# Optimization experiments

Hardware: AMD Instinct MI355X
Metric: run time of the kernel (lower is better)

Reference implementation:

```python
import jax, jax.numpy as jnp
import numpy as np

D_MODEL = 512
NUM_HEADS = 8


def setup_inputs() -> dict:
    key = jax.random.key(0)
    ks = jax.random.split(key, 12)
    B, S, D = 2, 4096, D_MODEL
    scale = 1.0 / np.sqrt(D)
    inp = {
        "q": jax.random.normal(ks[0], (B, S, D), jnp.float32),
        "k": jax.random.normal(ks[1], (B, S, D), jnp.float32),
        "v": jax.random.normal(ks[2], (B, S, D), jnp.float32),
        "w_q": jax.random.normal(ks[3], (D, D), jnp.float32) * scale,
        "b_q": jax.random.normal(ks[4], (D,), jnp.float32) * scale,
        "w_k": jax.random.normal(ks[5], (D, D), jnp.float32) * scale,
        "b_k": jax.random.normal(ks[6], (D,), jnp.float32) * scale,
        "w_v": jax.random.normal(ks[7], (D, D), jnp.float32) * scale,
        "b_v": jax.random.normal(ks[8], (D,), jnp.float32) * scale,
        "w_o": jax.random.normal(ks[9], (D, D), jnp.float32) * scale,
        "b_o": jax.random.normal(ks[10], (D,), jnp.float32) * scale,
    }
    return inp


def _split_heads(x, h):
    b, s, d = x.shape
    return x.reshape(b, s, h, d // h).transpose(0, 2, 1, 3)  # [B,H,S,dk]


def reference(q, k, v, w_q, b_q, w_k, b_k, w_v, b_v, w_o, b_o):
    h = NUM_HEADS
    # Linear projections (torch Linear: x @ W.T + b)
    qh = _split_heads(q @ w_q.T + b_q, h)
    kh = _split_heads(k @ w_k.T + b_k, h)
    vh = _split_heads(v @ w_v.T + b_v, h)
    d_k = kh.shape[-1]
    scores = jnp.einsum("bhsd,bhtd->bhst", qh, kh) / jnp.sqrt(jnp.float32(d_k))
    attn = jax.nn.softmax(scores, axis=-1)  # [B,H,S,S] - materialized, as in source
    out = jnp.einsum("bhst,bhtd->bhsd", attn, vh)
    b, _, s, dk = out.shape
    out = out.transpose(0, 2, 1, 3).reshape(b, s, h * dk)
    return out @ w_o.T + b_o
```

## Files before the change

### kernel.cpp

```cpp
#include <hip/hip_runtime.h>
#include <hip/hip_bf16.h>

#define D_MODEL 512
#define NHEAD   8
#define DK      64
#define SEQ     4096
#define BATCH   2
#define NTOK    (BATCH * SEQ)

typedef __bf16 bf16;
typedef __bf16 bf16x2 __attribute__((ext_vector_type(2)));
typedef __bf16 bf16x4 __attribute__((ext_vector_type(4)));
typedef __bf16 bf16x8 __attribute__((ext_vector_type(8)));
typedef float  f32x4  __attribute__((ext_vector_type(4)));
typedef float  f32x16 __attribute__((ext_vector_type(16)));
typedef unsigned u32x4 __attribute__((ext_vector_type(4)));

#define MFMA16(a, b, c) __builtin_amdgcn_mfma_f32_16x16x32_bf16((a), (b), (c), 0, 0, 0)
#define MFMA32(a, b, c) __builtin_amdgcn_mfma_f32_32x32x16_bf16((a), (b), (c), 0, 0, 0)

#define QSCALE 0.18033688f

__device__ __forceinline__ unsigned pkbf16(float a, float b) {
    bf16x2 t = {(bf16)a, (bf16)b};
    return __builtin_bit_cast(unsigned, t);
}

__device__ __forceinline__ void softmax_pack(const f32x16& sc, float& l,
                                             u32x4& pa, u32x4& pb) {
    float p0 = __builtin_amdgcn_exp2f(sc[0]);
    float p1 = __builtin_amdgcn_exp2f(sc[1]);
    float p2 = __builtin_amdgcn_exp2f(sc[2]);
    float p3 = __builtin_amdgcn_exp2f(sc[3]);
    l += (p0 + p1) + (p2 + p3);
    unsigned y0 = pkbf16(p0, p1), y1 = pkbf16(p2, p3);
    p0 = __builtin_amdgcn_exp2f(sc[4]);
    p1 = __builtin_amdgcn_exp2f(sc[5]);
    p2 = __builtin_amdgcn_exp2f(sc[6]);
    p3 = __builtin_amdgcn_exp2f(sc[7]);
    l += (p0 + p1) + (p2 + p3);
    unsigned y2 = pkbf16(p0, p1), y3 = pkbf16(p2, p3);
    auto s0 = __builtin_amdgcn_permlane32_swap(y0, y2, false, false);
    auto s1 = __builtin_amdgcn_permlane32_swap(y1, y3, false, false);
    pa[0] = s0[0]; pa[2] = s0[1]; pa[1] = s1[0]; pa[3] = s1[1];

    p0 = __builtin_amdgcn_exp2f(sc[8]);
    p1 = __builtin_amdgcn_exp2f(sc[9]);
    p2 = __builtin_amdgcn_exp2f(sc[10]);
    p3 = __builtin_amdgcn_exp2f(sc[11]);
    l += (p0 + p1) + (p2 + p3);
    y0 = pkbf16(p0, p1); y1 = pkbf16(p2, p3);
    p0 = __builtin_amdgcn_exp2f(sc[12]);
    p1 = __builtin_amdgcn_exp2f(sc[13]);
    p2 = __builtin_amdgcn_exp2f(sc[14]);
    p3 = __builtin_amdgcn_exp2f(sc[15]);
    l += (p0 + p1) + (p2 + p3);
    y2 = pkbf16(p0, p1); y3 = pkbf16(p2, p3);
    auto s2 = __builtin_amdgcn_permlane32_swap(y0, y2, false, false);
    auto s3 = __builtin_amdgcn_permlane32_swap(y1, y3, false, false);
    pb[0] = s2[0]; pb[2] = s2[1]; pb[1] = s3[0]; pb[3] = s3[1];
}

__global__ __launch_bounds__(256) void cvt_w(
    const float* __restrict__ wq, const float* __restrict__ wk,
    const float* __restrict__ wv, const float* __restrict__ wo,
    bf16* __restrict__ Wb)
{
    int i = blockIdx.x * 256 + threadIdx.x;
    int m = i >> 16;
    int g = i & 65535;
    const float* src = (m == 0) ? wq : (m == 1) ? wk : (m == 2) ? wv : wo;
    float4 x = *(const float4*)(src + (size_t)g * 4);
    bf16x4 y = {(bf16)x.x, (bf16)x.y, (bf16)x.z, (bf16)x.w};
    *(bf16x4*)(Wb + (size_t)m * D_MODEL * D_MODEL + (size_t)g * 4) = y;
}

__global__ __launch_bounds__(256, 3) void proj_qkv(
    const float* __restrict__ q, const float* __restrict__ k, const float* __restrict__ v,
    const bf16* __restrict__ Wb,
    const float* __restrict__ bq, const float* __restrict__ bk, const float* __restrict__ bv,
    bf16* __restrict__ Qh, bf16* __restrict__ Kh, bf16* __restrict__ Vt)
{
    const int p = blockIdx.z;
    const float* X    = (p == 0) ? q  : (p == 1) ? k  : v;
    const bf16*  W    = Wb + (size_t)p * D_MODEL * D_MODEL;
    const float* bias = (p == 0) ? bq : (p == 1) ? bk : bv;

    __shared__ union __align__(16) {
        struct { bf16 As[128][72]; bf16 Bs[128][72]; } g;
        bf16 T[128][136];
    } sm;

    const int m0   = blockIdx.x * 128;
    const int n0   = blockIdx.y * 128;
    const int tid  = threadIdx.x;
    const int lane = tid & 63;
    const int wave = tid >> 6;
    const int low4 = lane & 15;
    const int quad = lane >> 4;
    const int wm   = wave >> 1;
    const int wn   = wave & 1;

    int srow[8], sc4[8];
    for (int it = 0; it < 8; ++it) {
        int idx = tid + it * 256;
        srow[it] = idx >> 4;
        sc4[it]  = (idx & 15) * 4;
    }
    int br[4], bc[4];
    for (int it = 0; it < 4; ++it) {
        int idx = tid + it * 256;
        br[it] = idx >> 3;
        bc[it] = (idx & 7) * 8;
    }

    float4 gA[8];
    bf16x8 gB[4];
    for (int it = 0; it < 8; ++it)
        gA[it] = *(const float4*)(X + (size_t)(m0 + srow[it]) * D_MODEL + sc4[it]);
    for (int it = 0; it < 4; ++it)
        gB[it] = *(const bf16x8*)(W + (size_t)(n0 + br[it]) * D_MODEL + bc[it]);

    f32x4 acc[4][4];
    for (int i = 0; i < 4; ++i)
        for (int j = 0; j < 4; ++j)
            acc[i][j] = f32x4{0.f, 0.f, 0.f, 0.f};

    for (int k0 = 0; k0 < D_MODEL; k0 += 64) {
        __syncthreads();
        for (int it = 0; it < 8; ++it) {
            bf16x4 wa = {(bf16)gA[it].x, (bf16)gA[it].y, (bf16)gA[it].z, (bf16)gA[it].w};
            *(bf16x4*)&sm.g.As[srow[it]][sc4[it]] = wa;
        }
        for (int it = 0; it < 4; ++it)
            *(bf16x8*)&sm.g.Bs[br[it]][bc[it]] = gB[it];
        __syncthreads();

        if (k0 + 64 < D_MODEL) {
            for (int it = 0; it < 8; ++it)
                gA[it] = *(const float4*)(X + (size_t)(m0 + srow[it]) * D_MODEL + k0 + 64 + sc4[it]);
            for (int it = 0; it < 4; ++it)
                gB[it] = *(const bf16x8*)(W + (size_t)(n0 + br[it]) * D_MODEL + k0 + 64 + bc[it]);
        }

        for (int ks = 0; ks < 2; ++ks) {
            bf16x8 a[4], b[4];
            for (int i = 0; i < 4; ++i)
                a[i] = *(const bf16x8*)&sm.g.As[wm * 64 + i * 16 + low4][ks * 32 + quad * 8];
            for (int j = 0; j < 4; ++j)
                b[j] = *(const bf16x8*)&sm.g.Bs[wn * 64 + j * 16 + low4][ks * 32 + quad * 8];
            for (int i = 0; i < 4; ++i)
                for (int j = 0; j < 4; ++j)
                    acc[i][j] = MFMA16(a[i], b[j], acc[i][j]);
        }
    }

    if (p < 2) {
        bf16* Out = (p == 0) ? Qh : Kh;
        const float sc = (p == 0) ? QSCALE : 1.0f;
        for (int j = 0; j < 4; ++j) {
            int col = n0 + wn * 64 + j * 16 + low4;
            float bcol = bias[col];
            for (int i = 0; i < 4; ++i)
                for (int r = 0; r < 4; ++r) {
                    int row = m0 + wm * 64 + i * 16 + quad * 4 + r;
                    Out[(size_t)row * D_MODEL + col] = (bf16)((acc[i][j][r] + bcol) * sc);
                }
        }
    } else {
        __syncthreads();
        for (int j = 0; j < 4; ++j) {
            int col = n0 + wn * 64 + j * 16 + low4;
            float bcol = bias[col];
            for (int i = 0; i < 4; ++i)
                for (int r = 0; r < 4; ++r)
                    sm.T[wn * 64 + j * 16 + low4][wm * 64 + i * 16 + quad * 4 + r] =
                        (bf16)(acc[i][j][r] + bcol);
        }
        __syncthreads();
        const int bb = m0 >> 12;
        const int s0 = (m0 & 4095);
        for (int it = 0; it < 8; ++it) {
            int cc = it * 16 + (tid >> 4);
            int ml = (tid & 15) * 8;
            int col = n0 + cc;
            int hh = col >> 6, dd = col & 63;
            *(bf16x8*)&Vt[(((size_t)(bb * NHEAD + hh) * DK + dd) << 12) + s0 + ml] =
                *(const bf16x8*)&sm.T[cc][ml];
        }
    }
}

__global__ __launch_bounds__(512, 2) void attn(
    const bf16* __restrict__ Qh, const bf16* __restrict__ Kh,
    const bf16* __restrict__ Vt, bf16* __restrict__ O)
{
    __shared__ union __align__(16) {
        struct { bf16 Ks[2][128][72]; bf16 Vs[2][64][136]; } s;
        float Obuf[4][32][68];
    } sm;
    __shared__ float Lbuf[4][32];

    const int q0   = blockIdx.x * 256;
    const int bh   = blockIdx.y;
    const int b    = bh >> 3, h = bh & 7;
    const int tid  = threadIdx.x;
    const int lane = tid & 63;
    const int wave = tid >> 6;
    const int qg   = wave >> 1;
    const int kg   = wave & 1;
    const int m32  = lane & 31;
    const int hl   = lane >> 5;

    const bf16* Kbase = Kh + (size_t)b * SEQ * D_MODEL + h * DK;
    const bf16* Vbase = Vt + (size_t)bh * DK * SEQ;

    const bf16* Qrow0 = Qh + (size_t)(b * SEQ + q0 + qg * 64 + m32) * D_MODEL + h * DK;
    const bf16* Qrow1 = Qrow0 + (size_t)32 * D_MODEL;
    bf16x8 qf0[4], qf1[4];
#pragma unroll
    for (int ks = 0; ks < 4; ++ks) {
        qf0[ks] = *(const bf16x8*)(Qrow0 + ks * 16 + hl * 8);
        qf1[ks] = *(const bf16x8*)(Qrow1 + ks * 16 + hl * 8);
    }

    float l0 = 0.f, l1 = 0.f;
    f32x16 acc00, acc01, acc10, acc11;
#pragma unroll
    for (int i = 0; i < 16; ++i) {
        acc00[i] = 0.f; acc01[i] = 0.f; acc10[i] = 0.f; acc11[i] = 0.f;
    }

    int kr[2], kc[2], vr[2], vc[2];
#pragma unroll
    for (int it = 0; it < 2; ++it) {
        int c = tid + it * 512;
        kr[it] = c >> 3;  kc[it] = (c & 7) * 8;
        vr[it] = c >> 4;  vc[it] = (c & 15) * 8;
    }
    bf16x8 gk[2], gv[2];
#pragma unroll
    for (int it = 0; it < 2; ++it) {
        gk[it] = *(const bf16x8*)(Kbase + (size_t)kr[it] * D_MODEL + kc[it]);
        gv[it] = *(const bf16x8*)(Vbase + (size_t)vr[it] * SEQ + vc[it]);
    }
#pragma unroll
    for (int it = 0; it < 2; ++it) {
        *(bf16x8*)&sm.s.Ks[0][kr[it]][kc[it]] = gk[it];
        *(bf16x8*)&sm.s.Vs[0][vr[it]][vc[it]] = gv[it];
    }

    for (int t0 = 0; t0 < SEQ; t0 += 128) {
        const int cur = (t0 >> 7) & 1;
        const bool pf = (t0 + 128 < SEQ);

        if (pf) {
#pragma unroll
            for (int it = 0; it < 2; ++it) {
                gk[it] = *(const bf16x8*)(Kbase + (size_t)(t0 + 128 + kr[it]) * D_MODEL + kc[it]);
                gv[it] = *(const bf16x8*)(Vbase + (size_t)vr[it] * SEQ + t0 + 128 + vc[it]);
            }
        }

        __syncthreads();

        u32x4 pq0[4], pq1[4];
#pragma unroll
        for (int mt = 0; mt < 2; ++mt) {
            f32x16 s0, s1;
#pragma unroll
            for (int i = 0; i < 16; ++i) { s0[i] = 0.f; s1[i] = 0.f; }
            __builtin_amdgcn_s_setprio(1);
#pragma unroll
            for (int ks = 0; ks < 4; ++ks) {
                bf16x8 kf = *(const bf16x8*)&sm.s.Ks[cur][kg * 64 + mt * 32 + m32][ks * 16 + hl * 8];
                s0 = MFMA32(kf, qf0[ks], s0);
                s1 = MFMA32(kf, qf1[ks], s1);
            }
            __builtin_amdgcn_s_setprio(0);
            u32x4 a0, b0, a1, b1;
            softmax_pack(s0, l0, a0, b0);
            softmax_pack(s1, l1, a1, b1);
            pq0[2 * mt] = a0; pq0[2 * mt + 1] = b0;
            pq1[2 * mt] = a1; pq1[2 * mt + 1] = b1;
        }

        __builtin_amdgcn_s_setprio(1);
#pragma unroll
        for (int ksl = 0; ksl < 4; ++ksl) {
            bf16x8 pA = __builtin_bit_cast(bf16x8, pq0[ksl]);
            bf16x8 pB = __builtin_bit_cast(bf16x8, pq1[ksl]);
            bf16x8 v0 = *(const bf16x8*)&sm.s.Vs[cur][0 * 32 + m32][kg * 64 + ksl * 16 + hl * 8];
            acc00 = MFMA32(pA, v0, acc00);
            acc10 = MFMA32(pB, v0, acc10);
            bf16x8 v1 = *(const bf16x8*)&sm.s.Vs[cur][1 * 32 + m32][kg * 64 + ksl * 16 + hl * 8];
            acc01 = MFMA32(pA, v1, acc01);
            acc11 = MFMA32(pB, v1, acc11);
        }
        __builtin_amdgcn_s_setprio(0);

        if (pf) {
#pragma unroll
            for (int it = 0; it < 2; ++it) {
                *(bf16x8*)&sm.s.Ks[cur ^ 1][kr[it]][kc[it]] = gk[it];
                *(bf16x8*)&sm.s.Vs[cur ^ 1][vr[it]][vc[it]] = gv[it];
            }
        }
    }

    l0 += __shfl_xor(l0, 32);
    l1 += __shfl_xor(l1, 32);

#pragma unroll
    for (int qs = 0; qs < 2; ++qs) {
        float l = (qs == 0) ? l0 : l1;
        __syncthreads();
        if (kg == 1) {
#pragma unroll
            for (int r = 0; r < 16; ++r) {
                int qq = (r & 3) + 8 * (r >> 2) + 4 * hl;
                sm.Obuf[qg][qq][0 * 32 + m32] = (qs == 0) ? acc00[r] : acc10[r];
                sm.Obuf[qg][qq][1 * 32 + m32] = (qs == 0) ? acc01[r] : acc11[r];
            }
            if (hl == 0) Lbuf[qg][m32] = l;
        }
        __syncthreads();
        if (kg == 0) {
            float lt  = l + Lbuf[qg][m32];
            float inv = 1.0f / lt;
#pragma unroll
            for (int r = 0; r < 16; ++r) {
                int qq = (r & 3) + 8 * (r >> 2) + 4 * hl;
                float v0 = ((qs == 0) ? acc00[r] : acc10[r]) + sm.Obuf[qg][qq][0 * 32 + m32];
                float v1 = ((qs == 0) ? acc01[r] : acc11[r]) + sm.Obuf[qg][qq][1 * 32 + m32];
                float iv = __shfl(inv, qq);
                size_t row = (size_t)(b * SEQ + q0 + qg * 64 + qs * 32 + qq);
                O[row * D_MODEL + h * DK + 0 * 32 + m32] = (bf16)(v0 * iv);
                O[row * D_MODEL + h * DK + 1 * 32 + m32] = (bf16)(v1 * iv);
            }
        }
    }
}

__global__ __launch_bounds__(256, 4) void proj_out(
    const bf16* __restrict__ Oin, const bf16* __restrict__ Wo,
    const float* __restrict__ bo, float* __restrict__ out)
{
    __shared__ bf16 As[64][72];
    __shared__ bf16 Bs[64][72];

    const int m0   = blockIdx.x * 64;
    const int n0   = blockIdx.y * 64;
    const int tid  = threadIdx.x;
    const int lane = tid & 63;
    const int wave = tid >> 6;
    const int low4 = lane & 15;
    const int quad = lane >> 4;
    const int wm   = wave >> 1;
    const int wn   = wave & 1;

    int arow[2], ag[2];
    for (int it = 0; it < 2; ++it) {
        int idx = tid + it * 256;
        arow[it] = idx >> 3;
        ag[it]   = (idx & 7) * 8;
    }

    bf16x8 gA[2], gB[2];
    for (int it = 0; it < 2; ++it) {
        gA[it] = *(const bf16x8*)(Oin + (size_t)(m0 + arow[it]) * D_MODEL + ag[it]);
        gB[it] = *(const bf16x8*)(Wo + (size_t)(n0 + arow[it]) * D_MODEL + ag[it]);
    }

    f32x4 acc[2][2];
    for (int i = 0; i < 2; ++i)
        for (int j = 0; j < 2; ++j)
            acc[i][j] = f32x4{0.f, 0.f, 0.f, 0.f};

    for (int k0 = 0; k0 < D_MODEL; k0 += 64) {
        __syncthreads();
        for (int it = 0; it < 2; ++it) {
            *(bf16x8*)&As[arow[it]][ag[it]] = gA[it];
            *(bf16x8*)&Bs[arow[it]][ag[it]] = gB[it];
        }
        __syncthreads();

        if (k0 + 64 < D_MODEL) {
            for (int it = 0; it < 2; ++it) {
                gA[it] = *(const bf16x8*)(Oin + (size_t)(m0 + arow[it]) * D_MODEL + k0 + 64 + ag[it]);
                gB[it] = *(const bf16x8*)(Wo + (size_t)(n0 + arow[it]) * D_MODEL + k0 + 64 + ag[it]);
            }
        }

        for (int ks = 0; ks < 2; ++ks) {
            bf16x8 a[2], b[2];
            for (int i = 0; i < 2; ++i)
                a[i] = *(const bf16x8*)&As[wm * 32 + i * 16 + low4][ks * 32 + quad * 8];
            for (int j = 0; j < 2; ++j)
                b[j] = *(const bf16x8*)&Bs[wn * 32 + j * 16 + low4][ks * 32 + quad * 8];
            for (int i = 0; i < 2; ++i)
                for (int j = 0; j < 2; ++j)
                    acc[i][j] = MFMA16(a[i], b[j], acc[i][j]);
        }
    }

    for (int j = 0; j < 2; ++j) {
        int col = n0 + wn * 32 + j * 16 + low4;
        float bcol = bo[col];
        for (int i = 0; i < 2; ++i)
            for (int r = 0; r < 4; ++r) {
                int row = m0 + wm * 32 + i * 16 + quad * 4 + r;
                out[(size_t)row * D_MODEL + col] = acc[i][j][r] + bcol;
            }
    }
}

extern "C" void kernel_launch(void* const* d_in, const int* in_sizes, int n_in,
                              void* d_out, int out_size, void* d_ws, size_t ws_size,
                              hipStream_t stream)
{
    const float* q  = (const float*)d_in[0];
    const float* k  = (const float*)d_in[1];
    const float* v  = (const float*)d_in[2];
    const float* wq = (const float*)d_in[3];
    const float* bq = (const float*)d_in[4];
    const float* wk = (const float*)d_in[5];
    const float* bk = (const float*)d_in[6];
    const float* wv = (const float*)d_in[7];
    const float* bv = (const float*)d_in[8];
    const float* wo = (const float*)d_in[9];
    const float* bo = (const float*)d_in[10];

    const size_t NT = (size_t)NTOK * D_MODEL;
    bf16* Qh = (bf16*)d_ws;
    bf16* Kh = Qh + NT;
    bf16* Vt = Kh + NT;
    bf16* O  = Vt + NT;
    bf16* Wb = O + NT;

    cvt_w<<<1024, 256, 0, stream>>>(wq, wk, wv, wo, Wb);

    dim3 g1(NTOK / 128, D_MODEL / 128, 3);
    proj_qkv<<<g1, 256, 0, stream>>>(q, k, v, Wb, bq, bk, bv, Qh, Kh, Vt);

    dim3 g2(SEQ / 256, BATCH * NHEAD);
    attn<<<g2, 512, 0, stream>>>(Qh, Kh, Vt, O);

    dim3 g3(NTOK / 64, D_MODEL / 64);
    proj_out<<<g3, 256, 0, stream>>>(O, Wb + (size_t)3 * D_MODEL * D_MODEL, bo, (float*)d_out);
}
```

Measured before the change: 220.3 us.

## Software-pipeline PV MMA one tile behind QK with triple-buffered LDS

Restructures the attention main loop so the P·V MFMAs for the previous key tile run before the QK^T and softmax of the current tile, letting matrix work overlap softmax VALU work. K/V shared buffers go from double to triple so the previous V tile stays resident while the next is being filled, and a final epilogue drains the last PV step. Launch bounds drop to one 512-thread block per CU, since LDS usage and the extra live P registers grow. This risks lower occupancy and less latency hiding across blocks.

```diff
diff --git a/kernel.cpp b/kernel.cpp
--- a/kernel.cpp
+++ b/kernel.cpp
@@ -191,12 +191,12 @@
     }
 }
 
-__global__ __launch_bounds__(512, 2) void attn(
+__global__ __launch_bounds__(512, 1) void attn(
     const bf16* __restrict__ Qh, const bf16* __restrict__ Kh,
     const bf16* __restrict__ Vt, bf16* __restrict__ O)
 {
     __shared__ union __align__(16) {
-        struct { bf16 Ks[2][128][72]; bf16 Vs[2][64][136]; } s;
+        struct { bf16 Ks[3][128][72]; bf16 Vs[3][64][136]; } s;
         float Obuf[4][32][68];
     } sm;
     __shared__ float Lbuf[4][32];
@@ -231,6 +231,10 @@
         acc00[i] = 0.f; acc01[i] = 0.f; acc10[i] = 0.f; acc11[i] = 0.f;
     }
 
+    u32x4 pc0[4], pc1[4];
+#pragma unroll
+    for (int i = 0; i < 4; ++i) { pc0[i] = u32x4{0,0,0,0}; pc1[i] = u32x4{0,0,0,0}; }
+
     int kr[2], kc[2], vr[2], vc[2];
 #pragma unroll
     for (int it = 0; it < 2; ++it) {
@@ -250,9 +254,12 @@
         *(bf16x8*)&sm.s.Vs[0][vr[it]][vc[it]] = gv[it];
     }
 
+    int bi = 0;
     for (int t0 = 0; t0 < SEQ; t0 += 128) {
-        const int cur = (t0 >> 7) & 1;
-        const bool pf = (t0 + 128 < SEQ);
+        const int nbi = (bi == 2) ? 0 : bi + 1;
+        const int pbi = (bi == 0) ? 2 : bi - 1;
+        const bool pf    = (t0 + 128 < SEQ);
+        const bool first = (t0 == 0);
 
         if (pf) {
 #pragma unroll
@@ -264,7 +271,22 @@
 
         __syncthreads();
 
-        u32x4 pq0[4], pq1[4];
+        if (!first) {
+            __builtin_amdgcn_s_setprio(1);
+#pragma unroll
+            for (int ksl = 0; ksl < 4; ++ksl) {
+                bf16x8 pA = __builtin_bit_cast(bf16x8, pc0[ksl]);
+                bf16x8 pB = __builtin_bit_cast(bf16x8, pc1[ksl]);
+                bf16x8 v0 = *(const bf16x8*)&sm.s.Vs[pbi][0 * 32 + m32][kg * 64 + ksl * 16 + hl * 8];
+                acc00 = MFMA32(pA, v0, acc00);
+                acc10 = MFMA32(pB, v0, acc10);
+                bf16x8 v1 = *(const bf16x8*)&sm.s.Vs[pbi][1 * 32 + m32][kg * 64 + ksl * 16 + hl * 8];
+                acc01 = MFMA32(pA, v1, acc01);
+                acc11 = MFMA32(pB, v1, acc11);
+            }
+            __builtin_amdgcn_s_setprio(0);
+        }
+
 #pragma unroll
         for (int mt = 0; mt < 2; ++mt) {
             f32x16 s0, s1;
@@ -273,7 +295,7 @@
             __builtin_amdgcn_s_setprio(1);
 #pragma unroll
             for (int ks = 0; ks < 4; ++ks) {
-                bf16x8 kf = *(const bf16x8*)&sm.s.Ks[cur][kg * 64 + mt * 32 + m32][ks * 16 + hl * 8];
+                bf16x8 kf = *(const bf16x8*)&sm.s.Ks[bi][kg * 64 + mt * 32 + m32][ks * 16 + hl * 8];
                 s0 = MFMA32(kf, qf0[ks], s0);
                 s1 = MFMA32(kf, qf1[ks], s1);
             }
@@ -281,31 +303,35 @@
             u32x4 a0, b0, a1, b1;
             softmax_pack(s0, l0, a0, b0);
             softmax_pack(s1, l1, a1, b1);
-            pq0[2 * mt] = a0; pq0[2 * mt + 1] = b0;
-            pq1[2 * mt] = a1; pq1[2 * mt + 1] = b1;
-        }
-
+            pc0[2 * mt] = a0; pc0[2 * mt + 1] = b0;
+            pc1[2 * mt] = a1; pc1[2 * mt + 1] = b1;
+        }
+
+        if (pf) {
+#pragma unroll
+            for (int it = 0; it < 2; ++it) {
+                *(bf16x8*)&sm.s.Ks[nbi][kr[it]][kc[it]] = gk[it];
+                *(bf16x8*)&sm.s.Vs[nbi][vr[it]][vc[it]] = gv[it];
+            }
+        }
+        bi = nbi;
+    }
+
+    {
+        const int lbi = (bi == 0) ? 2 : bi - 1;
         __builtin_amdgcn_s_setprio(1);
 #pragma unroll
         for (int ksl = 0; ksl < 4; ++ksl) {
-            bf16x8 pA = __builtin_bit_cast(bf16x8, pq0[ksl]);
-            bf16x8 pB = __builtin_bit_cast(bf16x8, pq1[ksl]);
-            bf16x8 v0 = *(const bf16x8*)&sm.s.Vs[cur][0 * 32 + m32][kg * 64 + ksl * 16 + hl * 8];
+            bf16x8 pA = __builtin_bit_cast(bf16x8, pc0[ksl]);
+            bf16x8 pB = __builtin_bit_cast(bf16x8, pc1[ksl]);
+            bf16x8 v0 = *(const bf16x8*)&sm.s.Vs[lbi][0 * 32 + m32][kg * 64 + ksl * 16 + hl * 8];
             acc00 = MFMA32(pA, v0, acc00);
             acc10 = MFMA32(pB, v0, acc10);
-            bf16x8 v1 = *(const bf16x8*)&sm.s.Vs[cur][1 * 32 + m32][kg * 64 + ksl * 16 + hl * 8];
+            bf16x8 v1 = *(const bf16x8*)&sm.s.Vs[lbi][1 * 32 + m32][kg * 64 + ksl * 16 + hl * 8];
             acc01 = MFMA32(pA, v1, acc01);
             acc11 = MFMA32(pB, v1, acc11);
         }
         __builtin_amdgcn_s_setprio(0);
-
-        if (pf) {
-#pragma unroll
-            for (int it = 0; it < 2; ++it) {
-                *(bf16x8*)&sm.s.Ks[cur ^ 1][kr[it]][kc[it]] = gk[it];
-                *(bf16x8*)&sm.s.Vs[cur ^ 1][vr[it]][vc[it]] = gv[it];
-            }
-        }
     }
 
     l0 += __shfl_xor(l0, 32);
```

Measured after the change: 220.5 us. Within noise of the previous version (+0.1%).

## Pre-convert inputs to bf16 and use direct global-to-LDS loads in projections

Applied to the files above, without the earlier changes.

Adds a separate kernel that converts q/k/v activations to bf16 in the workspace. The projection GEMMs now load tiles straight into LDS with global_load_lds instead of staging through registers, and drop the register prefetch. proj_out is also widened to 128-column tiles. The LDS tiles lose their padding, so bank conflicts are possible, and without double buffering load latency is no longer hidden. The extra conversion pass adds a read of the fp32 inputs and a write of the bf16 copies.

```diff
diff --git a/kernel.cpp b/kernel.cpp
--- a/kernel.cpp
+++ b/kernel.cpp
@@ -15,11 +15,19 @@
 typedef float  f32x4  __attribute__((ext_vector_type(4)));
 typedef float  f32x16 __attribute__((ext_vector_type(16)));
 typedef unsigned u32x4 __attribute__((ext_vector_type(4)));
+typedef unsigned int u32;
 
 #define MFMA16(a, b, c) __builtin_amdgcn_mfma_f32_16x16x32_bf16((a), (b), (c), 0, 0, 0)
 #define MFMA32(a, b, c) __builtin_amdgcn_mfma_f32_32x32x16_bf16((a), (b), (c), 0, 0, 0)
 
 #define QSCALE 0.18033688f
+
+__device__ __forceinline__ void gll16(const bf16* g, bf16* l) {
+    __builtin_amdgcn_global_load_lds(
+        (const __attribute__((address_space(1))) u32*)g,
+        (__attribute__((address_space(3))) u32*)l,
+        16, 0, 0);
+}
 
 __device__ __forceinline__ unsigned pkbf16(float a, float b) {
     bf16x2 t = {(bf16)a, (bf16)b};
@@ -75,19 +83,30 @@
     *(bf16x4*)(Wb + (size_t)m * D_MODEL * D_MODEL + (size_t)g * 4) = y;
 }
 
+__global__ __launch_bounds__(256) void cvt_x(
+    const float* __restrict__ q, const float* __restrict__ k,
+    const float* __restrict__ v, bf16* __restrict__ Xb)
+{
+    int z = blockIdx.y;
+    int i = blockIdx.x * 256 + threadIdx.x;
+    const float* src = (z == 0) ? q : (z == 1) ? k : v;
+    float4 x = *(const float4*)(src + (size_t)i * 4);
+    bf16x4 y = {(bf16)x.x, (bf16)x.y, (bf16)x.z, (bf16)x.w};
+    *(bf16x4*)(Xb + (size_t)z * NTOK * D_MODEL + (size_t)i * 4) = y;
+}
+
 __global__ __launch_bounds__(256, 3) void proj_qkv(
-    const float* __restrict__ q, const float* __restrict__ k, const float* __restrict__ v,
-    const bf16* __restrict__ Wb,
+    const bf16* __restrict__ Xb, const bf16* __restrict__ Wb,
     const float* __restrict__ bq, const float* __restrict__ bk, const float* __restrict__ bv,
     bf16* __restrict__ Qh, bf16* __restrict__ Kh, bf16* __restrict__ Vt)
 {
     const int p = blockIdx.z;
-    const float* X    = (p == 0) ? q  : (p == 1) ? k  : v;
-    const bf16*  W    = Wb + (size_t)p * D_MODEL * D_MODEL;
+    const bf16* X = Xb + (size_t)p * NTOK * D_MODEL;
+    const bf16* W = Wb + (size_t)p * D_MODEL * D_MODEL;
     const float* bias = (p == 0) ? bq : (p == 1) ? bk : bv;
 
     __shared__ union __align__(16) {
-        struct { bf16 As[128][72]; bf16 Bs[128][72]; } g;
+        struct { bf16 A[128 * 64]; bf16 B[128 * 64]; } g;
         bf16 T[128][136];
     } sm;
 
@@ -101,78 +120,67 @@
     const int wm   = wave >> 1;
     const int wn   = wave & 1;
 
-    int srow[8], sc4[8];
-    for (int it = 0; it < 8; ++it) {
-        int idx = tid + it * 256;
-        srow[it] = idx >> 4;
-        sc4[it]  = (idx & 15) * 4;
-    }
-    int br[4], bc[4];
-    for (int it = 0; it < 4; ++it) {
-        int idx = tid + it * 256;
-        br[it] = idx >> 3;
-        bc[it] = (idx & 7) * 8;
-    }
-
-    float4 gA[8];
-    bf16x8 gB[4];
-    for (int it = 0; it < 8; ++it)
-        gA[it] = *(const float4*)(X + (size_t)(m0 + srow[it]) * D_MODEL + sc4[it]);
-    for (int it = 0; it < 4; ++it)
-        gB[it] = *(const bf16x8*)(W + (size_t)(n0 + br[it]) * D_MODEL + bc[it]);
-
     f32x4 acc[4][4];
+#pragma unroll
     for (int i = 0; i < 4; ++i)
+#pragma unroll
         for (int j = 0; j < 4; ++j)
             acc[i][j] = f32x4{0.f, 0.f, 0.f, 0.f};
 
     for (int k0 = 0; k0 < D_MODEL; k0 += 64) {
-        __syncthreads();
-        for (int it = 0; it < 8; ++it) {
-            bf16x4 wa = {(bf16)gA[it].x, (bf16)gA[it].y, (bf16)gA[it].z, (bf16)gA[it].w};
-            *(bf16x4*)&sm.g.As[srow[it]][sc4[it]] = wa;
-        }
-        for (int it = 0; it < 4; ++it)
-            *(bf16x8*)&sm.g.Bs[br[it]][bc[it]] = gB[it];
-        __syncthreads();
-
-        if (k0 + 64 < D_MODEL) {
-            for (int it = 0; it < 8; ++it)
-                gA[it] = *(const float4*)(X + (size_t)(m0 + srow[it]) * D_MODEL + k0 + 64 + sc4[it]);
-            for (int it = 0; it < 4; ++it)
-                gB[it] = *(const bf16x8*)(W + (size_t)(n0 + br[it]) * D_MODEL + k0 + 64 + bc[it]);
-        }
-
+#pragma unroll
+        for (int ps = 0; ps < 4; ++ps) {
+            int s   = ps * 256 + tid;
+            int row = s >> 3;
+            int c   = (s & 7) * 8;
+            bf16* la = sm.g.A + (size_t)(ps * 256 + wave * 64) * 8;
+            bf16* lb = sm.g.B + (size_t)(ps * 256 + wave * 64) * 8;
+            gll16(X + (size_t)(m0 + row) * D_MODEL + k0 + c, la);
+            gll16(W + (size_t)(n0 + row) * D_MODEL + k0 + c, lb);
+        }
+        __syncthreads();
+
+#pragma unroll
         for (int ks = 0; ks < 2; ++ks) {
             bf16x8 a[4], b[4];
+#pragma unroll
             for (int i = 0; i < 4; ++i)
-                a[i] = *(const bf16x8*)&sm.g.As[wm * 64 + i * 16 + low4][ks * 32 + quad * 8];
+                a[i] = *(const bf16x8*)&sm.g.A[(size_t)(wm * 64 + i * 16 + low4) * 64 + ks * 32 + quad * 8];
+#pragma unroll
             for (int j = 0; j < 4; ++j)
-                b[j] = *(const bf16x8*)&sm.g.Bs[wn * 64 + j * 16 + low4][ks * 32 + quad * 8];
+                b[j] = *(const bf16x8*)&sm.g.B[(size_t)(wn * 64 + j * 16 + low4) * 64 + ks * 32 + quad * 8];
+#pragma unroll
             for (int i = 0; i < 4; ++i)
+#pragma unroll
                 for (int j = 0; j < 4; ++j)
                     acc[i][j] = MFMA16(a[i], b[j], acc[i][j]);
         }
+        __syncthreads();
     }
 
     if (p < 2) {
         bf16* Out = (p == 0) ? Qh : Kh;
         const float sc = (p == 0) ? QSCALE : 1.0f;
+#pragma unroll
         for (int j = 0; j < 4; ++j) {
             int col = n0 + wn * 64 + j * 16 + low4;
             float bcol = bias[col];
+#pragma unroll
             for (int i = 0; i < 4; ++i)
+#pragma unroll
                 for (int r = 0; r < 4; ++r) {
                     int row = m0 + wm * 64 + i * 16 + quad * 4 + r;
                     Out[(size_t)row * D_MODEL + col] = (bf16)((acc[i][j][r] + bcol) * sc);
                 }
         }
     } else {
-        __syncthreads();
+#pragma unroll
         for (int j = 0; j < 4; ++j) {
             int col = n0 + wn * 64 + j * 16 + low4;
             float bcol = bias[col];
+#pragma unroll
             for (int i = 0; i < 4; ++i)
+#pragma unroll
                 for (int r = 0; r < 4; ++r)
                     sm.T[wn * 64 + j * 16 + low4][wm * 64 + i * 16 + quad * 4 + r] =
                         (bf16)(acc[i][j][r] + bcol);
@@ -180,6 +188,7 @@
         __syncthreads();
         const int bb = m0 >> 12;
         const int s0 = (m0 & 4095);
+#pragma unroll
         for (int it = 0; it < 8; ++it) {
             int cc = it * 16 + (tid >> 4);
             int ml = (tid & 15) * 8;
@@ -346,11 +355,11 @@
     const bf16* __restrict__ Oin, const bf16* __restrict__ Wo,
     const float* __restrict__ bo, float* __restrict__ out)
 {
-    __shared__ bf16 As[64][72];
-    __shared__ bf16 Bs[64][72];
+    __shared__ __align__(16) bf16 As[64 * 64];
+    __shared__ __align__(16) bf16 Bs[128 * 64];
 
     const int m0   = blockIdx.x * 64;
-    const int n0   = blockIdx.y * 64;
+    const int n0   = blockIdx.y * 128;
     const int tid  = threadIdx.x;
     const int lane = tid & 63;
     const int wave = tid >> 6;
@@ -359,55 +368,57 @@
     const int wm   = wave >> 1;
     const int wn   = wave & 1;
 
-    int arow[2], ag[2];
-    for (int it = 0; it < 2; ++it) {
-        int idx = tid + it * 256;
-        arow[it] = idx >> 3;
-        ag[it]   = (idx & 7) * 8;
-    }
-
-    bf16x8 gA[2], gB[2];
-    for (int it = 0; it < 2; ++it) {
-        gA[it] = *(const bf16x8*)(Oin + (size_t)(m0 + arow[it]) * D_MODEL + ag[it]);
-        gB[it] = *(const bf16x8*)(Wo + (size_t)(n0 + arow[it]) * D_MODEL + ag[it]);
-    }
-
-    f32x4 acc[2][2];
+    f32x4 acc[2][4];
+#pragma unroll
     for (int i = 0; i < 2; ++i)
-        for (int j = 0; j < 2; ++j)
+#pragma unroll
+        for (int j = 0; j < 4; ++j)
             acc[i][j] = f32x4{0.f, 0.f, 0.f, 0.f};
 
     for (int k0 = 0; k0 < D_MODEL; k0 += 64) {
-        __syncthreads();
-        for (int it = 0; it < 2; ++it) {
-            *(bf16x8*)&As[arow[it]][ag[it]] = gA[it];
-            *(bf16x8*)&Bs[arow[it]][ag[it]] = gB[it];
-        }
-        __syncthreads();
-
-        if (k0 + 64 < D_MODEL) {
-            for (int it = 0; it < 2; ++it) {
-                gA[it] = *(const bf16x8*)(Oin + (size_t)(m0 + arow[it]) * D_MODEL + k0 + 64 + ag[it]);
-                gB[it] = *(const bf16x8*)(Wo + (size_t)(n0 + arow[it]) * D_MODEL + k0 + 64 + ag[it]);
-            }
-        }
-
+#pragma unroll
+        for (int ps = 0; ps < 2; ++ps) {
+            int s   = ps * 256 + tid;
+            int row = s >> 3;
+            int c   = (s & 7) * 8;
+            bf16* la = As + (size_t)(ps * 256 + wave * 64) * 8;
+            gll16(Oin + (size_t)(m0 + row) * D_MODEL + k0 + c, la);
+        }
+#pragma unroll
+        for (int ps = 0; ps < 4; ++ps) {
+            int s   = ps * 256 + tid;
+            int row = s >> 3;
+            int c   = (s & 7) * 8;
+            bf16* lb = Bs + (size_t)(ps * 256 + wave * 64) * 8;
+            gll16(Wo + (size_t)(n0 + row) * D_MODEL + k0 + c, lb);
+        }
+        __syncthreads();
+
+#pragma unroll
         for (int ks = 0; ks < 2; ++ks) {
-            bf16x8 a[2], b[2];
+            bf16x8 a[2], b[4];
+#pragma unroll
             for (int i = 0; i < 2; ++i)
-                a[i] = *(const bf16x8*)&As[wm * 32 + i * 16 + low4][ks * 32 + quad * 8];
-            for (int j = 0; j < 2; ++j)
-                b[j] = *(const bf16x8*)&Bs[wn * 32 + j * 16 + low4][ks * 32 + quad * 8];
+                a[i] = *(const bf16x8*)&As[(size_t)(wm * 32 + i * 16 + low4) * 64 + ks * 32 + quad * 8];
+#pragma unroll
+            for (int j = 0; j < 4; ++j)
+                b[j] = *(const bf16x8*)&Bs[(size_t)(wn * 64 + j * 16 + low4) * 64 + ks * 32 + quad * 8];
+#pragma unroll
             for (int i = 0; i < 2; ++i)
-                for (int j = 0; j < 2; ++j)
+#pragma unroll
+                for (int j = 0; j < 4; ++j)
                     acc[i][j] = MFMA16(a[i], b[j], acc[i][j]);
         }
-    }
-
-    for (int j = 0; j < 2; ++j) {
-        int col = n0 + wn * 32 + j * 16 + low4;
+        __syncthreads();
+    }
+
+#pragma unroll
+    for (int j = 0; j < 4; ++j) {
+        int col = n0 + wn * 64 + j * 16 + low4;
         float bcol = bo[col];
+#pragma unroll
         for (int i = 0; i < 2; ++i)
+#pragma unroll
             for (int r = 0; r < 4; ++r) {
                 int row = m0 + wm * 32 + i * 16 + quad * 4 + r;
                 out[(size_t)row * D_MODEL + col] = acc[i][j][r] + bcol;
@@ -437,15 +448,19 @@
     bf16* Vt = Kh + NT;
     bf16* O  = Vt + NT;
     bf16* Wb = O + NT;
+    bf16* Xb = Wb + (size_t)4 * D_MODEL * D_MODEL;
 
     cvt_w<<<1024, 256, 0, stream>>>(wq, wk, wv, wo, Wb);
 
+    dim3 gx(4096, 3);
+    cvt_x<<<gx, 256, 0, stream>>>(q, k, v, Xb);
+
     dim3 g1(NTOK / 128, D_MODEL / 128, 3);
-    proj_qkv<<<g1, 256, 0, stream>>>(q, k, v, Wb, bq, bk, bv, Qh, Kh, Vt);
+    proj_qkv<<<g1, 256, 0, stream>>>(Xb, Wb, bq, bk, bv, Qh, Kh, Vt);
 
     dim3 g2(SEQ / 256, BATCH * NHEAD);
     attn<<<g2, 512, 0, stream>>>(Qh, Kh, Vt, O);
 
-    dim3 g3(NTOK / 64, D_MODEL / 64);
+    dim3 g3(NTOK / 64, D_MODEL / 128);
     proj_out<<<g3, 256, 0, stream>>>(O, Wb + (size_t)3 * D_MODEL * D_MODEL, bo, (float*)d_out);
 }
```

New measurement: 214.0 us. 1.03x faster.
